# Kernel optimization log

Measured on AMD Instinct MI355X. Metric: run time of the kernel, lower is better.

## Reference

```python
import jax, jax.numpy as jnp
import numpy as np

N, D, E_EDGES = 50000, 128, 800000
HEADS, REL_DIM, N_RELS, LAYERS = 4, 64, 64, 2
HD = HEADS * D  # per-head out_channels == d_model (concat=False)
LN_EPS = 1e-5
NEG_SLOPE = 0.2


def setup_inputs() -> dict:
    key = jax.random.key(0)
    ks = jax.random.split(key, 12)
    s = 0.02
    return {
        "x_flat": jax.random.normal(ks[0], (N, D), jnp.float32),
        "edge_index": jax.random.randint(ks[1], (2, E_EDGES), 0, N, jnp.int32),
        "edge_type": jax.random.randint(ks[2], (E_EDGES,), 0, N_RELS, jnp.int32),
        "rel_emb": jax.random.normal(ks[3], (N_RELS, REL_DIM), jnp.float32) * s,
        # stacked params for LAYERS GATv2Conv layers
        "Wl": jax.random.normal(ks[4], (LAYERS, D, HD), jnp.float32) * s,
        "bl": jnp.zeros((LAYERS, HD), jnp.float32),
        "Wr": jax.random.normal(ks[5], (LAYERS, D, HD), jnp.float32) * s,
        "br": jnp.zeros((LAYERS, HD), jnp.float32),
        "We": jax.random.normal(ks[6], (LAYERS, REL_DIM, HD), jnp.float32) * s,
        "att": jax.random.normal(ks[7], (LAYERS, HEADS, D), jnp.float32) * s,
        "b_out": jnp.zeros((LAYERS, D), jnp.float32),
        "ln_g": jnp.ones((LAYERS, D), jnp.float32),
        "ln_b": jnp.zeros((LAYERS, D), jnp.float32),
    }


def _gatv2_layer(h, src, dst, eattr, Wl, bl, Wr, br, We, att, b_out):
    # h: [N, D] -> per-head transforms [N, H, C]
    xl = (h @ Wl + bl).reshape(N, HEADS, D)   # source transform (messages)
    xr = (h @ Wr + br).reshape(N, HEADS, D)   # target transform
    xe = (eattr @ We).reshape(-1, HEADS, D)   # edge transform (no bias, PyG)
    # GATv2 attention: a^T leaky_relu(xl_j + xr_i + xe)
    s = jax.nn.leaky_relu(xl[src] + xr[dst] + xe, NEG_SLOPE)  # [E, H, C]
    logits = jnp.einsum('ehc,hc->eh', s, att)                  # [E, H]
    # segment softmax over destination nodes
    mx = jax.ops.segment_max(logits, dst, num_segments=N)      # [N, H]
    ex = jnp.exp(logits - mx[dst])
    den = jax.ops.segment_sum(ex, dst, num_segments=N)
    alpha = ex / den[dst]                                      # [E, H]
    msg = xl[src] * alpha[..., None]                           # [E, H, C]
    out = jax.ops.segment_sum(msg.reshape(-1, HD), dst, num_segments=N)
    out = out.reshape(N, HEADS, D).mean(axis=1) + b_out        # concat=False -> mean
    return out


def _layernorm(x, g, b):
    mu = x.mean(-1, keepdims=True)
    var = ((x - mu) ** 2).mean(-1, keepdims=True)
    return (x - mu) * jax.lax.rsqrt(var + LN_EPS) * g + b


def reference(x_flat, edge_index, edge_type, rel_emb, Wl, bl, Wr, br, We, att, b_out, ln_g, ln_b):
    src, dst = edge_index[0], edge_index[1]
    eattr = rel_emb[edge_type]  # [E, REL_DIM]
    h = x_flat
    for l in range(LAYERS):
        m = _gatv2_layer(h, src, dst, eattr, Wl[l], bl[l], Wr[l], br[l], We[l], att[l], b_out[l])
        m = jax.nn.gelu(m, approximate=False)  # dropout in eval mode
        h = _layernorm(h + m, ln_g[l], ln_b[l])
    return h
```

## Files before the change

kernel.cpp:

```cpp
#include <hip/hip_runtime.h>
#include <hip/hip_bf16.h>

#define NN 50000
#define DM 128
#define EE 800000
#define NH 4
#define HDIM 512
#define NRELS 64
#define RDIM 64
#define LAYERS 2
#define NB 196

#define PM_HB 6250
#define PM_WC 1024
#define PM_XE 256
#define PM_CZ 196
#define PM_TOT (PM_HB + PM_WC + PM_XE + PM_CZ + 1)

typedef short frag8 __attribute__((ext_vector_type(8)));
typedef float f32x4 __attribute__((ext_vector_type(4)));
typedef float f32x2 __attribute__((ext_vector_type(2)));

__device__ __forceinline__ float b2f(unsigned short u) {
    unsigned v = ((unsigned)u) << 16;
    union { unsigned u; float f; } c; c.u = v; return c.f;
}
__device__ __forceinline__ float b2f_lo(unsigned u) {
    union { unsigned u; float f; } c; c.u = u << 16; return c.f;
}
__device__ __forceinline__ float b2f_hi(unsigned u) {
    union { unsigned u; float f; } c; c.u = u & 0xFFFF0000u; return c.f;
}
__device__ __forceinline__ float b2f_hi_raw(unsigned u) {
    union { unsigned u; float f; } c; c.u = u; return c.f;
}
__device__ __forceinline__ unsigned short f2b(float f) {
    union { float f; unsigned u; } c; c.f = f;
    unsigned u = c.u;
    u += 0x7FFFu + ((u >> 16) & 1u);
    return (unsigned short)(u >> 16);
}

template<int CTRL>
__device__ __forceinline__ float dpp_add(float x) {
    int yi = __builtin_amdgcn_update_dpp(0, __builtin_bit_cast(int, x),
                                         CTRL, 0xF, 0xF, true);
    return x + __builtin_bit_cast(float, yi);
}

__global__ void count_kernel(const int* __restrict__ dst, int* __restrict__ counts) {
    int e = blockIdx.x * 256 + threadIdx.x;
    if (e < EE) atomicAdd(&counts[dst[e]], 1);
}

__global__ __launch_bounds__(256) void psum_kernel(const int* __restrict__ counts,
                                                   int* __restrict__ psums) {
    int idx = blockIdx.x * 256 + threadIdx.x;
    int x = (idx < NN) ? counts[idx] : 0;
    int lane = threadIdx.x & 63, wv = threadIdx.x >> 6;
    #pragma unroll
    for (int d = 1; d < 64; d <<= 1) x += __shfl_xor(x, d, 64);
    __shared__ int ws[4];
    if (lane == 0) ws[wv] = x;
    __syncthreads();
    if (threadIdx.x == 0) psums[blockIdx.x] = ws[0] + ws[1] + ws[2] + ws[3];
}

__global__ __launch_bounds__(256) void pscan_kernel(const int* __restrict__ psums,
                                                    int* __restrict__ offs,
                                                    int* __restrict__ row_ptr) {
    int t = threadIdx.x;
    int x = (t < NB) ? psums[t] : 0;
    int lane = t & 63, wv = t >> 6;
    int incl = x;
    #pragma unroll
    for (int d = 1; d < 64; d <<= 1) {
        int y = __shfl_up(incl, d, 64);
        if (lane >= d) incl += y;
    }
    __shared__ int ws[4];
    if (lane == 63) ws[wv] = incl;
    __syncthreads();
    int off = 0;
    for (int k = 0; k < wv; ++k) off += ws[k];
    if (t < NB) offs[t] = incl + off - x;
    if (t == 0) row_ptr[0] = 0;
}

__global__ __launch_bounds__(256) void pfin_kernel(const int* __restrict__ counts,
                                                   const int* __restrict__ offs,
                                                   int* __restrict__ row_ptr,
                                                   int* __restrict__ cursor) {
    int idx = blockIdx.x * 256 + threadIdx.x;
    int x = (idx < NN) ? counts[idx] : 0;
    int lane = threadIdx.x & 63, wv = threadIdx.x >> 6;
    int incl = x;
    #pragma unroll
    for (int d = 1; d < 64; d <<= 1) {
        int y = __shfl_up(incl, d, 64);
        if (lane >= d) incl += y;
    }
    __shared__ int ws[4];
    if (lane == 63) ws[wv] = incl;
    __syncthreads();
    int off = offs[blockIdx.x];
    for (int k = 0; k < wv; ++k) off += ws[k];
    if (idx < NN) {
        int v = off + incl;
        row_ptr[idx + 1] = v;
        cursor[idx] = v - x;
    }
}

__global__ void scatter_pk_kernel(const int* __restrict__ ei, const int* __restrict__ etype,
                                  int* __restrict__ cursor, uint2* __restrict__ pkq) {
    int e = blockIdx.x * 256 + threadIdx.x;
    if (e < EE) {
        int d = ei[EE + e];
        int p = atomicAdd(&cursor[d], 1);
        uint2 v;
        v.x = (unsigned)ei[e] << 10;
        v.y = (unsigned)etype[e] << 10;
        pkq[p] = v;
    }
}

__global__ __launch_bounds__(256) void prep_misc_kernel(
    const float* __restrict__ x_flat,
    const float* __restrict__ Wl, const float* __restrict__ Wr,
    const float* __restrict__ rel_emb, const float* __restrict__ We,
    const float* __restrict__ att,
    unsigned short* __restrict__ hb, unsigned short* __restrict__ Wt,
    unsigned short* __restrict__ xeb, float* __restrict__ be,
    int* __restrict__ counts) {
    int b = blockIdx.x, t = threadIdx.x;
    if (b < PM_HB) {
        int idx = b * 256 + t;
        float4 v = ((const float4*)x_flat)[idx];
        ushort4 o;
        o.x = f2b(v.x); o.y = f2b(v.y); o.z = f2b(v.z); o.w = f2b(v.w);
        ((ushort4*)hb)[idx] = o;
        return;
    }
    b -= PM_HB;
    if (b < PM_WC) {
        int idx = b * 256 + t;
        int m = idx >> 16;
        int r = idx & 65535;
        int c = r >> 7, k = r & 127;
        int l = m >> 1;
        const float* W = (m & 1) ? Wr : Wl;
        Wt[idx] = f2b(W[(size_t)l * DM * HDIM + k * HDIM + c]);
        return;
    }
    b -= PM_WC;
    if (b < PM_XE) {
        int idx = b * 256 + t;
        int l  = idx / (NRELS * HDIM);
        int r  = (idx / HDIM) & (NRELS - 1);
        int hc = idx & (HDIM - 1);
        const float* Wel = We + (size_t)l * RDIM * HDIM;
        float s = 0.f;
        #pragma unroll 8
        for (int d = 0; d < RDIM; ++d) s += rel_emb[r * RDIM + d] * Wel[d * HDIM + hc];
        xeb[idx] = f2b(s);
        return;
    }
    b -= PM_XE;
    if (b < PM_CZ) {
        int idx = b * 256 + t;
        if (idx < NN) counts[idx] = 0;
        return;
    }
    __shared__ float aw_s[LAYERS * NH * RDIM];
    #pragma unroll
    for (int k = 0; k < 2; ++k) {
        int idx = t * 2 + k;
        int l = idx >> 8, h = (idx >> 6) & 3, d = idx & 63;
        const float* ap = att + (size_t)l * HDIM + h * DM;
        const float* wp = We + (size_t)l * RDIM * HDIM + (size_t)d * HDIM + h * DM;
        float s = 0.f;
        #pragma unroll 8
        for (int c = 0; c < DM; ++c) s += ap[c] * wp[c];
        aw_s[idx] = s;
    }
    __syncthreads();
    #pragma unroll
    for (int k = 0; k < 2; ++k) {
        int idx = t * 2 + k;
        int l = idx >> 8, r = (idx >> 2) & 63, h = idx & 3;
        const float* rp = rel_emb + r * RDIM;
        const float* ap = aw_s + l * 256 + h * 64;
        float s = 0.f;
        #pragma unroll 8
        for (int d = 0; d < RDIM; ++d) s += rp[d] * ap[d];
        be[idx] = 0.6f * s;
    }
}

__global__ __launch_bounds__(256) void gemm_xlxr_ab_kernel(
    const unsigned short* __restrict__ hb,
    const unsigned short* __restrict__ WtL,
    const unsigned short* __restrict__ WtR,
    const float* __restrict__ bl, const float* __restrict__ br,
    const float* __restrict__ att_l,
    unsigned short* __restrict__ xl, unsigned short* __restrict__ xr,
    float* __restrict__ ab) {
    int w = threadIdx.x >> 6, lane = threadIdx.x & 63;
    int m0 = blockIdx.x * 64;
    int colL = lane & 15, kg = lane >> 4;

    frag8 a[4][4];
    #pragma unroll
    for (int mt = 0; mt < 4; ++mt) {
        int row = m0 + mt * 16 + colL;
        if (row >= NN) row = NN - 1;
        const unsigned short* arow = hb + (size_t)row * DM;
        #pragma unroll
        for (int kc = 0; kc < 4; ++kc) {
            uint4 raw = *(const uint4*)(arow + kc * 32 + kg * 8);
            a[mt][kc] = __builtin_bit_cast(frag8, raw);
        }
    }

    float prow[4][2][4];
    #pragma unroll
    for (int mt = 0; mt < 4; ++mt)
        #pragma unroll
        for (int mat = 0; mat < 2; ++mat)
            #pragma unroll
            for (int r = 0; r < 4; ++r) prow[mt][mat][r] = 0.f;

    #pragma unroll
    for (int mat = 0; mat < 2; ++mat) {
        const unsigned short* Wt = mat ? WtR : WtL;
        const float* bias = mat ? br : bl;
        unsigned short* out = mat ? xr : xl;
        #pragma unroll
        for (int nt = 0; nt < 8; ++nt) {
            int col = w * 128 + nt * 16 + colL;
            f32x4 acc[4];
            #pragma unroll
            for (int mt = 0; mt < 4; ++mt) acc[mt] = f32x4{0.f, 0.f, 0.f, 0.f};
            #pragma unroll
            for (int kc = 0; kc < 4; ++kc) {
                uint4 raw = *(const uint4*)(Wt + (size_t)col * DM + kc * 32 + kg * 8);
                frag8 b = __builtin_bit_cast(frag8, raw);
                #pragma unroll
                for (int mt = 0; mt < 4; ++mt)
                    acc[mt] = __builtin_amdgcn_mfma_f32_16x16x32_bf16(a[mt][kc], b, acc[mt], 0, 0, 0);
            }
            float bb = bias[col];
            float ac = att_l[col];
            #pragma unroll
            for (int mt = 0; mt < 4; ++mt) {
                #pragma unroll
                for (int r = 0; r < 4; ++r) {
                    float v = acc[mt][r] + bb;
                    int row = m0 + mt * 16 + kg * 4 + r;
                    if (row < NN) out[(size_t)row * HDIM + col] = f2b(v);
                    prow[mt][mat][r] = fmaf(ac, v, prow[mt][mat][r]);
                }
            }
        }
    }
    #pragma unroll
    for (int d = 1; d < 16; d <<= 1) {
        #pragma unroll
        for (int mt = 0; mt < 4; ++mt)
            #pragma unroll
            for (int mat = 0; mat < 2; ++mat)
                #pragma unroll
                for (int r = 0; r < 4; ++r)
                    prow[mt][mat][r] += __shfl_xor(prow[mt][mat][r], d, 64);
    }
    if (colL == 0) {
        #pragma unroll
        for (int mt = 0; mt < 4; ++mt) {
            int row = m0 + mt * 16 + kg * 4;
            #pragma unroll
            for (int mat = 0; mat < 2; ++mat)
                #pragma unroll
                for (int r = 0; r < 4; ++r)
                    if (row + r < NN)
                        ab[(size_t)(row + r) * 8 + mat * 4 + w] = 0.6f * prow[mt][mat][r];
        }
    }
}

__global__ __launch_bounds__(256) void node_fused_kernel(
    const int* __restrict__ row_ptr,
    const uint2* __restrict__ pkq,
    const unsigned short* __restrict__ xl,
    const unsigned short* __restrict__ xr,
    const unsigned short* __restrict__ xeb_l,
    const float* __restrict__ ab,
    const float* __restrict__ be_l,
    const float* __restrict__ att_l,
    const float* __restrict__ h_in,
    const float* __restrict__ b_out, const float* __restrict__ ln_g,
    const float* __restrict__ ln_b,
    float* __restrict__ h_out,
    unsigned short* __restrict__ hb_out) {
    int w = threadIdx.x >> 6, l = threadIdx.x & 63;
    int i = blockIdx.x * 4 + w;
    int hh = l >> 4;
    __shared__ float cl[4][64][4];
    __shared__ uint2 pk_s[4][64];

    int beg = row_ptr[i], end = row_ptr[i + 1];
    int c0 = (l & 15) * 8;

    uint4 xrv = *(const uint4*)(xr + (size_t)i * HDIM + l * 8);
    f32x2 xrp0 = f32x2{b2f_lo(xrv.x), b2f_hi(xrv.x)};
    f32x2 xrp1 = f32x2{b2f_lo(xrv.y), b2f_hi(xrv.y)};
    f32x2 xrp2 = f32x2{b2f_lo(xrv.z), b2f_hi(xrv.z)};
    f32x2 xrp3 = f32x2{b2f_lo(xrv.w), b2f_hi(xrv.w)};
    float4 at0 = ((const float4*)(att_l + l * 8))[0];
    float4 at1 = ((const float4*)(att_l + l * 8))[1];
    float atv[8] = {at0.x * 0.4f, at0.y * 0.4f, at0.z * 0.4f, at0.w * 0.4f,
                    at1.x * 0.4f, at1.y * 0.4f, at1.z * 0.4f, at1.w * 0.4f};
    float4 bxv = ((const float4*)ab)[2 * i + 1];
    float4 hv0 = *(const float4*)(h_in + (size_t)i * DM + c0);
    float4 hv1 = *(const float4*)(h_in + (size_t)i * DM + c0 + 4);

    const char* xl_b = (const char*)xl;
    const char* xe_b = (const char*)xeb_l;
    uint l16 = (uint)l << 4;

    float ss = 0.f;
    f32x2 acc0 = f32x2{0.f, 0.f}, acc1 = f32x2{0.f, 0.f};
    f32x2 acc2 = f32x2{0.f, 0.f}, acc3 = f32x2{0.f, 0.f};

    for (int cb = beg; cb < end; cb += 64) {
        int mc = min(64, end - cb);
        if (l < mc) {
            uint2 pk = pkq[cb + l];
            pk_s[w][l] = pk;
            int s = pk.x >> 10, r = pk.y >> 10;
            float4 a4 = ((const float4*)ab)[2 * s];
            float4 b4 = ((const float4*)be_l)[r];
            cl[w][l][0] = a4.x + b4.x + bxv.x;
            cl[w][l][1] = a4.y + b4.y + bxv.y;
            cl[w][l][2] = a4.z + b4.z + bxv.z;
            cl[w][l][3] = a4.w + b4.w + bxv.w;
        }
        uint2 pk0 = pk_s[w][0];
        uint4 vvP = *(const uint4*)(xl_b + pk0.x + l16);
        uint4 eeP = *(const uint4*)(xe_b + pk0.y + l16);
        float cjP = cl[w][0][hh];
        for (int j = 1; j <= mc; ++j) {
            uint4 vv = vvP; uint4 ee = eeP; float cj = cjP;
            if (j < mc) {
                uint2 pkj = pk_s[w][j];
                vvP = *(const uint4*)(xl_b + pkj.x + l16);
                eeP = *(const uint4*)(xe_b + pkj.y + l16);
                cjP = cl[w][j][hh];
            }
            f32x2 xp0 = f32x2{b2f_lo(vv.x), b2f_hi_raw(vv.x)};
            f32x2 xp1 = f32x2{b2f_lo(vv.y), b2f_hi_raw(vv.y)};
            f32x2 xp2 = f32x2{b2f_lo(vv.z), b2f_hi_raw(vv.z)};
            f32x2 xp3 = f32x2{b2f_lo(vv.w), b2f_hi_raw(vv.w)};
            f32x2 z0 = (xp0 + xrp0) + f32x2{b2f_lo(ee.x), b2f_hi_raw(ee.x)};
            f32x2 z1 = (xp1 + xrp1) + f32x2{b2f_lo(ee.y), b2f_hi_raw(ee.y)};
            f32x2 z2 = (xp2 + xrp2) + f32x2{b2f_lo(ee.z), b2f_hi_raw(ee.z)};
            f32x2 z3 = (xp3 + xrp3) + f32x2{b2f_lo(ee.w), b2f_hi_raw(ee.w)};
            float partial = fmaf(atv[0], fabsf(z0[0]),
                            fmaf(atv[1], fabsf(z0[1]),
                            fmaf(atv[2], fabsf(z1[0]),
                            fmaf(atv[3], fabsf(z1[1]),
                            fmaf(atv[4], fabsf(z2[0]),
                            fmaf(atv[5], fabsf(z2[1]),
                            fmaf(atv[6], fabsf(z3[0]), atv[7] * fabsf(z3[1]))))))));
            partial = dpp_add<0xB1>(partial);
            partial = dpp_add<0x4E>(partial);
            partial = dpp_add<0x124>(partial);
            partial = dpp_add<0x128>(partial);
            float we = __expf(partial + cj);
            ss += we;
            f32x2 wv = f32x2{we, we};
            acc0 += wv * xp0;
            acc1 += wv * xp1;
            acc2 += wv * xp2;
            acc3 += wv * xp3;
        }
    }

    float invs = (ss > 0.f) ? 1.f / ss : 0.f;
    float sv[8] = {acc0[0] * invs, acc0[1] * invs, acc1[0] * invs, acc1[1] * invs,
                   acc2[0] * invs, acc2[1] * invs, acc3[0] * invs, acc3[1] * invs};
    #pragma unroll
    for (int d = 16; d < 64; d <<= 1)
        #pragma unroll
        for (int k = 0; k < 8; ++k) sv[k] += __shfl_xor(sv[k], d, 64);

    float4 bo0 = *(const float4*)(b_out + c0);
    float4 bo1 = *(const float4*)(b_out + c0 + 4);
    float bov[8] = {bo0.x, bo0.y, bo0.z, bo0.w, bo1.x, bo1.y, bo1.z, bo1.w};
    float hvv[8] = {hv0.x, hv0.y, hv0.z, hv0.w, hv1.x, hv1.y, hv1.z, hv1.w};
    float yv[8];
    float la = 0.f, lb = 0.f;
    #pragma unroll
    for (int k = 0; k < 8; ++k) {
        float o = sv[k] * 0.25f + bov[k];
        float ge = 0.5f * o * (1.f + erff(o * 0.70710678118654752f));
        float y = hvv[k] + ge;
        yv[k] = y; la += y; lb += y * y;
    }
    la = dpp_add<0xB1>(la); la = dpp_add<0x4E>(la);
    la = dpp_add<0x124>(la); la = dpp_add<0x128>(la);
    lb = dpp_add<0xB1>(lb); lb = dpp_add<0x4E>(lb);
    lb = dpp_add<0x124>(lb); lb = dpp_add<0x128>(lb);
    float mean = la * (1.f / 128.f);
    float var = lb * (1.f / 128.f) - mean * mean;
    float rs = rsqrtf(var + 1e-5f);

    if (l < 16) {
        float4 g0 = *(const float4*)(ln_g + c0);
        float4 g1 = *(const float4*)(ln_g + c0 + 4);
        float4 q0 = *(const float4*)(ln_b + c0);
        float4 q1 = *(const float4*)(ln_b + c0 + 4);
        float gv[8] = {g0.x, g0.y, g0.z, g0.w, g1.x, g1.y, g1.z, g1.w};
        float qv[8] = {q0.x, q0.y, q0.z, q0.w, q1.x, q1.y, q1.z, q1.w};
        float ov[8];
        #pragma unroll
        for (int k = 0; k < 8; ++k)
            ov[k] = (yv[k] - mean) * rs * gv[k] + qv[k];
        float* hop = h_out + (size_t)i * DM + c0;
        *(float4*)hop = make_float4(ov[0], ov[1], ov[2], ov[3]);
        *(float4*)(hop + 4) = make_float4(ov[4], ov[5], ov[6], ov[7]);
        uint4 ob;
        ob.x = (unsigned)f2b(ov[0]) | ((unsigned)f2b(ov[1]) << 16);
        ob.y = (unsigned)f2b(ov[2]) | ((unsigned)f2b(ov[3]) << 16);
        ob.z = (unsigned)f2b(ov[4]) | ((unsigned)f2b(ov[5]) << 16);
        ob.w = (unsigned)f2b(ov[6]) | ((unsigned)f2b(ov[7]) << 16);
        *(uint4*)(hb_out + (size_t)i * DM + c0) = ob;
    }
}

extern "C" void kernel_launch(void* const* d_in, const int* in_sizes, int n_in,
                              void* d_out, int out_size, void* d_ws, size_t ws_size,
                              hipStream_t stream) {
    const float* x_flat   = (const float*)d_in[0];
    const int*   edge_idx = (const int*)d_in[1];
    const int*   edge_ty  = (const int*)d_in[2];
    const float* rel_emb  = (const float*)d_in[3];
    const float* Wl       = (const float*)d_in[4];
    const float* bl       = (const float*)d_in[5];
    const float* Wr       = (const float*)d_in[6];
    const float* br       = (const float*)d_in[7];
    const float* We       = (const float*)d_in[8];
    const float* att      = (const float*)d_in[9];
    const float* b_out    = (const float*)d_in[10];
    const float* ln_g     = (const float*)d_in[11];
    const float* ln_b     = (const float*)d_in[12];

    char* p = (char*)d_ws;
    auto carve = [&](size_t bytes) {
        void* r = (void*)p;
        p += (bytes + 255) & ~(size_t)255;
        return r;
    };
    unsigned short* xl     = (unsigned short*)carve((size_t)NN * HDIM * 2);
    unsigned short* xr     = (unsigned short*)carve((size_t)NN * HDIM * 2);
    float*          h1     = (float*)carve((size_t)NN * DM * 4);
    unsigned short* hb     = (unsigned short*)carve((size_t)NN * DM * 2);
    unsigned short* Wt     = (unsigned short*)carve((size_t)4 * DM * HDIM * 2);
    unsigned short* xeb    = (unsigned short*)carve((size_t)LAYERS * NRELS * HDIM * 2);
    float*          ab     = (float*)carve((size_t)NN * 8 * 4);
    float*          be     = (float*)carve((size_t)LAYERS * NRELS * NH * 4);
    int*            row_ptr= (int*)carve((size_t)(NN + 1) * 4);
    int*            counts = (int*)carve((size_t)NN * 4);
    int*            cursor = (int*)carve((size_t)NN * 4);
    int*            psums  = (int*)carve((size_t)NB * 4);
    int*            offs   = (int*)carve((size_t)NB * 4);
    uint2*          pkq    = (uint2*)carve((size_t)EE * 8);

    const int* dst = edge_idx + EE;

    prep_misc_kernel<<<PM_TOT, 256, 0, stream>>>(
        x_flat, Wl, Wr, rel_emb, We, att, hb, Wt, xeb, be, counts);

    count_kernel<<<(EE + 255) / 256, 256, 0, stream>>>(dst, counts);
    psum_kernel<<<NB, 256, 0, stream>>>(counts, psums);
    pscan_kernel<<<1, 256, 0, stream>>>(psums, offs, row_ptr);
    pfin_kernel<<<NB, 256, 0, stream>>>(counts, offs, row_ptr, cursor);
    scatter_pk_kernel<<<(EE + 255) / 256, 256, 0, stream>>>(edge_idx, edge_ty, cursor, pkq);

    const float* h_cur = x_flat;
    for (int l = 0; l < LAYERS; ++l) {
        float* h_next = (l == LAYERS - 1) ? (float*)d_out : h1;
        gemm_xlxr_ab_kernel<<<(NN + 63) / 64, 256, 0, stream>>>(
            hb,
            Wt + (size_t)(l * 2 + 0) * DM * HDIM,
            Wt + (size_t)(l * 2 + 1) * DM * HDIM,
            bl + (size_t)l * HDIM, br + (size_t)l * HDIM,
            att + (size_t)l * HDIM,
            xl, xr, ab);
        node_fused_kernel<<<NN / 4, 256, 0, stream>>>(
            row_ptr, pkq, xl, xr,
            xeb + (size_t)l * NRELS * HDIM,
            ab, be + (size_t)l * NRELS * NH,
            att + (size_t)l * HDIM,
            h_cur,
            b_out + (size_t)l * DM, ln_g + (size_t)l * DM, ln_b + (size_t)l * DM,
            h_next, hb);
        h_cur = h_next;
    }
}
```

Before: 606.3 us.

## Use persistent atomic work-queue for node kernel and halve GEMM row tile

The fused node kernel becomes persistent: 2048 blocks pull node indices from a global atomic counter, one per wavefront, instead of one block per four nodes. Per-layer counters are zeroed in the prep kernel, and per-column constants are hoisted out of the node loop. This targets load imbalance from uneven in-degrees and per-block launch overhead, at the cost of one atomic per node. The XL/XR GEMM also drops from 64 to 32 rows per block, doubling its grid to raise occupancy and cut register pressure, while reloading weights more often.

```diff
diff --git a/kernel.cpp b/kernel.cpp
--- a/kernel.cpp
+++ b/kernel.cpp
@@ -132,7 +132,7 @@
     const float* __restrict__ att,
     unsigned short* __restrict__ hb, unsigned short* __restrict__ Wt,
     unsigned short* __restrict__ xeb, float* __restrict__ be,
-    int* __restrict__ counts) {
+    int* __restrict__ counts, int* __restrict__ ctr) {
     int b = blockIdx.x, t = threadIdx.x;
     if (b < PM_HB) {
         int idx = b * 256 + t;
@@ -172,6 +172,7 @@
         if (idx < NN) counts[idx] = 0;
         return;
     }
+    if (t < 2) ctr[t] = 0;
     __shared__ float aw_s[LAYERS * NH * RDIM];
     #pragma unroll
     for (int k = 0; k < 2; ++k) {
@@ -207,12 +208,12 @@
     unsigned short* __restrict__ xl, unsigned short* __restrict__ xr,
     float* __restrict__ ab) {
     int w = threadIdx.x >> 6, lane = threadIdx.x & 63;
-    int m0 = blockIdx.x * 64;
+    int m0 = blockIdx.x * 32;
     int colL = lane & 15, kg = lane >> 4;
 
-    frag8 a[4][4];
-    #pragma unroll
-    for (int mt = 0; mt < 4; ++mt) {
+    frag8 a[2][4];
+    #pragma unroll
+    for (int mt = 0; mt < 2; ++mt) {
         int row = m0 + mt * 16 + colL;
         if (row >= NN) row = NN - 1;
         const unsigned short* arow = hb + (size_t)row * DM;
@@ -223,9 +224,9 @@
         }
     }
 
-    float prow[4][2][4];
-    #pragma unroll
-    for (int mt = 0; mt < 4; ++mt)
+    float prow[2][2][4];
+    #pragma unroll
+    for (int mt = 0; mt < 2; ++mt)
         #pragma unroll
         for (int mat = 0; mat < 2; ++mat)
             #pragma unroll
@@ -239,35 +240,34 @@
         #pragma unroll
         for (int nt = 0; nt < 8; ++nt) {
             int col = w * 128 + nt * 16 + colL;
-            f32x4 acc[4];
-            #pragma unroll
-            for (int mt = 0; mt < 4; ++mt) acc[mt] = f32x4{0.f, 0.f, 0.f, 0.f};
+            f32x4 acc0 = {0.f, 0.f, 0.f, 0.f};
+            f32x4 acc1 = {0.f, 0.f, 0.f, 0.f};
             #pragma unroll
             for (int kc = 0; kc < 4; ++kc) {
                 uint4 raw = *(const uint4*)(Wt + (size_t)col * DM + kc * 32 + kg * 8);
                 frag8 b = __builtin_bit_cast(frag8, raw);
-                #pragma unroll
-                for (int mt = 0; mt < 4; ++mt)
-                    acc[mt] = __builtin_amdgcn_mfma_f32_16x16x32_bf16(a[mt][kc], b, acc[mt], 0, 0, 0);
+                acc0 = __builtin_amdgcn_mfma_f32_16x16x32_bf16(a[0][kc], b, acc0, 0, 0, 0);
+                acc1 = __builtin_amdgcn_mfma_f32_16x16x32_bf16(a[1][kc], b, acc1, 0, 0, 0);
             }
             float bb = bias[col];
             float ac = att_l[col];
             #pragma unroll
-            for (int mt = 0; mt < 4; ++mt) {
-                #pragma unroll
-                for (int r = 0; r < 4; ++r) {
-                    float v = acc[mt][r] + bb;
-                    int row = m0 + mt * 16 + kg * 4 + r;
-                    if (row < NN) out[(size_t)row * HDIM + col] = f2b(v);
-                    prow[mt][mat][r] = fmaf(ac, v, prow[mt][mat][r]);
-                }
+            for (int r = 0; r < 4; ++r) {
+                float v0 = acc0[r] + bb;
+                float v1 = acc1[r] + bb;
+                int row0 = m0 + kg * 4 + r;
+                int row1 = row0 + 16;
+                if (row0 < NN) out[(size_t)row0 * HDIM + col] = f2b(v0);
+                if (row1 < NN) out[(size_t)row1 * HDIM + col] = f2b(v1);
+                prow[0][mat][r] = fmaf(ac, v0, prow[0][mat][r]);
+                prow[1][mat][r] = fmaf(ac, v1, prow[1][mat][r]);
             }
         }
     }
     #pragma unroll
     for (int d = 1; d < 16; d <<= 1) {
         #pragma unroll
-        for (int mt = 0; mt < 4; ++mt)
+        for (int mt = 0; mt < 2; ++mt)
             #pragma unroll
             for (int mat = 0; mat < 2; ++mat)
                 #pragma unroll
@@ -276,7 +276,7 @@
     }
     if (colL == 0) {
         #pragma unroll
-        for (int mt = 0; mt < 4; ++mt) {
+        for (int mt = 0; mt < 2; ++mt) {
             int row = m0 + mt * 16 + kg * 4;
             #pragma unroll
             for (int mat = 0; mat < 2; ++mat)
@@ -301,140 +301,149 @@
     const float* __restrict__ b_out, const float* __restrict__ ln_g,
     const float* __restrict__ ln_b,
     float* __restrict__ h_out,
-    unsigned short* __restrict__ hb_out) {
+    unsigned short* __restrict__ hb_out,
+    int* __restrict__ ctr) {
     int w = threadIdx.x >> 6, l = threadIdx.x & 63;
-    int i = blockIdx.x * 4 + w;
     int hh = l >> 4;
     __shared__ float cl[4][64][4];
     __shared__ uint2 pk_s[4][64];
 
-    int beg = row_ptr[i], end = row_ptr[i + 1];
     int c0 = (l & 15) * 8;
 
-    uint4 xrv = *(const uint4*)(xr + (size_t)i * HDIM + l * 8);
-    f32x2 xrp0 = f32x2{b2f_lo(xrv.x), b2f_hi(xrv.x)};
-    f32x2 xrp1 = f32x2{b2f_lo(xrv.y), b2f_hi(xrv.y)};
-    f32x2 xrp2 = f32x2{b2f_lo(xrv.z), b2f_hi(xrv.z)};
-    f32x2 xrp3 = f32x2{b2f_lo(xrv.w), b2f_hi(xrv.w)};
     float4 at0 = ((const float4*)(att_l + l * 8))[0];
     float4 at1 = ((const float4*)(att_l + l * 8))[1];
     float atv[8] = {at0.x * 0.4f, at0.y * 0.4f, at0.z * 0.4f, at0.w * 0.4f,
                     at1.x * 0.4f, at1.y * 0.4f, at1.z * 0.4f, at1.w * 0.4f};
-    float4 bxv = ((const float4*)ab)[2 * i + 1];
-    float4 hv0 = *(const float4*)(h_in + (size_t)i * DM + c0);
-    float4 hv1 = *(const float4*)(h_in + (size_t)i * DM + c0 + 4);
+    float4 bo0 = *(const float4*)(b_out + c0);
+    float4 bo1 = *(const float4*)(b_out + c0 + 4);
+    float bov[8] = {bo0.x, bo0.y, bo0.z, bo0.w, bo1.x, bo1.y, bo1.z, bo1.w};
+    float4 g0 = *(const float4*)(ln_g + c0);
+    float4 g1 = *(const float4*)(ln_g + c0 + 4);
+    float4 q0 = *(const float4*)(ln_b + c0);
+    float4 q1 = *(const float4*)(ln_b + c0 + 4);
 
     const char* xl_b = (const char*)xl;
     const char* xe_b = (const char*)xeb_l;
     uint l16 = (uint)l << 4;
 
-    float ss = 0.f;
-    f32x2 acc0 = f32x2{0.f, 0.f}, acc1 = f32x2{0.f, 0.f};
-    f32x2 acc2 = f32x2{0.f, 0.f}, acc3 = f32x2{0.f, 0.f};
-
-    for (int cb = beg; cb < end; cb += 64) {
-        int mc = min(64, end - cb);
-        if (l < mc) {
-            uint2 pk = pkq[cb + l];
-            pk_s[w][l] = pk;
-            int s = pk.x >> 10, r = pk.y >> 10;
-            float4 a4 = ((const float4*)ab)[2 * s];
-            float4 b4 = ((const float4*)be_l)[r];
-            cl[w][l][0] = a4.x + b4.x + bxv.x;
-            cl[w][l][1] = a4.y + b4.y + bxv.y;
-            cl[w][l][2] = a4.z + b4.z + bxv.z;
-            cl[w][l][3] = a4.w + b4.w + bxv.w;
+    for (;;) {
+        int i = 0;
+        if (l == 0) i = atomicAdd(ctr, 1);
+        i = __shfl(i, 0, 64);
+        if (i >= NN) break;
+
+        int beg = row_ptr[i], end = row_ptr[i + 1];
+
+        uint4 xrv = *(const uint4*)(xr + (size_t)i * HDIM + l * 8);
+        f32x2 xrp0 = f32x2{b2f_lo(xrv.x), b2f_hi(xrv.x)};
+        f32x2 xrp1 = f32x2{b2f_lo(xrv.y), b2f_hi(xrv.y)};
+        f32x2 xrp2 = f32x2{b2f_lo(xrv.z), b2f_hi(xrv.z)};
+        f32x2 xrp3 = f32x2{b2f_lo(xrv.w), b2f_hi(xrv.w)};
+        float4 bxv = ((const float4*)ab)[2 * i + 1];
+        float4 hv0 = *(const float4*)(h_in + (size_t)i * DM + c0);
+        float4 hv1 = *(const float4*)(h_in + (size_t)i * DM + c0 + 4);
+
+        float ss = 0.f;
+        f32x2 acc0 = f32x2{0.f, 0.f}, acc1 = f32x2{0.f, 0.f};
+        f32x2 acc2 = f32x2{0.f, 0.f}, acc3 = f32x2{0.f, 0.f};
+
+        for (int cb = beg; cb < end; cb += 64) {
+            int mc = min(64, end - cb);
+            if (l < mc) {
+                uint2 pk = pkq[cb + l];
+                pk_s[w][l] = pk;
+                int s = pk.x >> 10, r = pk.y >> 10;
+                float4 a4 = ((const float4*)ab)[2 * s];
+                float4 b4 = ((const float4*)be_l)[r];
+                cl[w][l][0] = a4.x + b4.x + bxv.x;
+                cl[w][l][1] = a4.y + b4.y + bxv.y;
+                cl[w][l][2] = a4.z + b4.z + bxv.z;
+                cl[w][l][3] = a4.w + b4.w + bxv.w;
+            }
+            uint2 pk0 = pk_s[w][0];
+            uint4 vvP = *(const uint4*)(xl_b + pk0.x + l16);
+            uint4 eeP = *(const uint4*)(xe_b + pk0.y + l16);
+            float cjP = cl[w][0][hh];
+            for (int j = 1; j <= mc; ++j) {
+                uint4 vv = vvP; uint4 ee = eeP; float cj = cjP;
+                if (j < mc) {
+                    uint2 pkj = pk_s[w][j];
+                    vvP = *(const uint4*)(xl_b + pkj.x + l16);
+                    eeP = *(const uint4*)(xe_b + pkj.y + l16);
+                    cjP = cl[w][j][hh];
+                }
+                f32x2 xp0 = f32x2{b2f_lo(vv.x), b2f_hi_raw(vv.x)};
+                f32x2 xp1 = f32x2{b2f_lo(vv.y), b2f_hi_raw(vv.y)};
+                f32x2 xp2 = f32x2{b2f_lo(vv.z), b2f_hi_raw(vv.z)};
+                f32x2 xp3 = f32x2{b2f_lo(vv.w), b2f_hi_raw(vv.w)};
+                f32x2 z0 = (xp0 + xrp0) + f32x2{b2f_lo(ee.x), b2f_hi_raw(ee.x)};
+                f32x2 z1 = (xp1 + xrp1) + f32x2{b2f_lo(ee.y), b2f_hi_raw(ee.y)};
+                f32x2 z2 = (xp2 + xrp2) + f32x2{b2f_lo(ee.z), b2f_hi_raw(ee.z)};
+                f32x2 z3 = (xp3 + xrp3) + f32x2{b2f_lo(ee.w), b2f_hi_raw(ee.w)};
+                float partial = fmaf(atv[0], fabsf(z0[0]),
+                                fmaf(atv[1], fabsf(z0[1]),
+                                fmaf(atv[2], fabsf(z1[0]),
+                                fmaf(atv[3], fabsf(z1[1]),
+                                fmaf(atv[4], fabsf(z2[0]),
+                                fmaf(atv[5], fabsf(z2[1]),
+                                fmaf(atv[6], fabsf(z3[0]), atv[7] * fabsf(z3[1]))))))));
+                partial = dpp_add<0xB1>(partial);
+                partial = dpp_add<0x4E>(partial);
+                partial = dpp_add<0x124>(partial);
+                partial = dpp_add<0x128>(partial);
+                float we = __expf(partial + cj);
+                ss += we;
+                f32x2 wv = f32x2{we, we};
+                acc0 += wv * xp0;
+                acc1 += wv * xp1;
+                acc2 += wv * xp2;
+                acc3 += wv * xp3;
+            }
         }
-        uint2 pk0 = pk_s[w][0];
-        uint4 vvP = *(const uint4*)(xl_b + pk0.x + l16);
-        uint4 eeP = *(const uint4*)(xe_b + pk0.y + l16);
-        float cjP = cl[w][0][hh];
-        for (int j = 1; j <= mc; ++j) {
-            uint4 vv = vvP; uint4 ee = eeP; float cj = cjP;
-            if (j < mc) {
-                uint2 pkj = pk_s[w][j];
-                vvP = *(const uint4*)(xl_b + pkj.x + l16);
-                eeP = *(const uint4*)(xe_b + pkj.y + l16);
-                cjP = cl[w][j][hh];
-            }
-            f32x2 xp0 = f32x2{b2f_lo(vv.x), b2f_hi_raw(vv.x)};
-            f32x2 xp1 = f32x2{b2f_lo(vv.y), b2f_hi_raw(vv.y)};
-            f32x2 xp2 = f32x2{b2f_lo(vv.z), b2f_hi_raw(vv.z)};
-            f32x2 xp3 = f32x2{b2f_lo(vv.w), b2f_hi_raw(vv.w)};
-            f32x2 z0 = (xp0 + xrp0) + f32x2{b2f_lo(ee.x), b2f_hi_raw(ee.x)};
-            f32x2 z1 = (xp1 + xrp1) + f32x2{b2f_lo(ee.y), b2f_hi_raw(ee.y)};
-            f32x2 z2 = (xp2 + xrp2) + f32x2{b2f_lo(ee.z), b2f_hi_raw(ee.z)};
-            f32x2 z3 = (xp3 + xrp3) + f32x2{b2f_lo(ee.w), b2f_hi_raw(ee.w)};
-            float partial = fmaf(atv[0], fabsf(z0[0]),
-                            fmaf(atv[1], fabsf(z0[1]),
-                            fmaf(atv[2], fabsf(z1[0]),
-                            fmaf(atv[3], fabsf(z1[1]),
-                            fmaf(atv[4], fabsf(z2[0]),
-                            fmaf(atv[5], fabsf(z2[1]),
-                            fmaf(atv[6], fabsf(z3[0]), atv[7] * fabsf(z3[1]))))))));
-            partial = dpp_add<0xB1>(partial);
-            partial = dpp_add<0x4E>(partial);
-            partial = dpp_add<0x124>(partial);
-            partial = dpp_add<0x128>(partial);
-            float we = __expf(partial + cj);
-            ss += we;
-            f32x2 wv = f32x2{we, we};
-            acc0 += wv * xp0;
-            acc1 += wv * xp1;
-            acc2 += wv * xp2;
-            acc3 += wv * xp3;
+
+        float invs = (ss > 0.f) ? 1.f / ss : 0.f;
+        float sv[8] = {acc0[0] * invs, acc0[1] * invs, acc1[0] * invs, acc1[1] * invs,
+                       acc2[0] * invs, acc2[1] * invs, acc3[0] * invs, acc3[1] * invs};
+        #pragma unroll
+        for (int d = 16; d < 64; d <<= 1)
+            #pragma unroll
+            for (int k = 0; k < 8; ++k) sv[k] += __shfl_xor(sv[k], d, 64);
+
+        float hvv[8] = {hv0.x, hv0.y, hv0.z, hv0.w, hv1.x, hv1.y, hv1.z, hv1.w};
+        float yv[8];
+        float la = 0.f, lb = 0.f;
+        #pragma unroll
+        for (int k = 0; k < 8; ++k) {
+            float o = sv[k] * 0.25f + bov[k];
+            float ge = 0.5f * o * (1.f + erff(o * 0.70710678118654752f));
+            float y = hvv[k] + ge;
+            yv[k] = y; la += y; lb += y * y;
         }
-    }
-
-    float invs = (ss > 0.f) ? 1.f / ss : 0.f;
-    float sv[8] = {acc0[0] * invs, acc0[1] * invs, acc1[0] * invs, acc1[1] * invs,
-                   acc2[0] * invs, acc2[1] * invs, acc3[0] * invs, acc3[1] * invs};
-    #pragma unroll
-    for (int d = 16; d < 64; d <<= 1)
-        #pragma unroll
-        for (int k = 0; k < 8; ++k) sv[k] += __shfl_xor(sv[k], d, 64);
-
-    float4 bo0 = *(const float4*)(b_out + c0);
-    float4 bo1 = *(const float4*)(b_out + c0 + 4);
-    float bov[8] = {bo0.x, bo0.y, bo0.z, bo0.w, bo1.x, bo1.y, bo1.z, bo1.w};
-    float hvv[8] = {hv0.x, hv0.y, hv0.z, hv0.w, hv1.x, hv1.y, hv1.z, hv1.w};
-    float yv[8];
-    float la = 0.f, lb = 0.f;
-    #pragma unroll
-    for (int k = 0; k < 8; ++k) {
-        float o = sv[k] * 0.25f + bov[k];
-        float ge = 0.5f * o * (1.f + erff(o * 0.70710678118654752f));
-        float y = hvv[k] + ge;
-        yv[k] = y; la += y; lb += y * y;
-    }
-    la = dpp_add<0xB1>(la); la = dpp_add<0x4E>(la);
-    la = dpp_add<0x124>(la); la = dpp_add<0x128>(la);
-    lb = dpp_add<0xB1>(lb); lb = dpp_add<0x4E>(lb);
-    lb = dpp_add<0x124>(lb); lb = dpp_add<0x128>(lb);
-    float mean = la * (1.f / 128.f);
-    float var = lb * (1.f / 128.f) - mean * mean;
-    float rs = rsqrtf(var + 1e-5f);
-
-    if (l < 16) {
-        float4 g0 = *(const float4*)(ln_g + c0);
-        float4 g1 = *(const float4*)(ln_g + c0 + 4);
-        float4 q0 = *(const float4*)(ln_b + c0);
-        float4 q1 = *(const float4*)(ln_b + c0 + 4);
-        float gv[8] = {g0.x, g0.y, g0.z, g0.w, g1.x, g1.y, g1.z, g1.w};
-        float qv[8] = {q0.x, q0.y, q0.z, q0.w, q1.x, q1.y, q1.z, q1.w};
-        float ov[8];
-        #pragma unroll
-        for (int k = 0; k < 8; ++k)
-            ov[k] = (yv[k] - mean) * rs * gv[k] + qv[k];
-        float* hop = h_out + (size_t)i * DM + c0;
-        *(float4*)hop = make_float4(ov[0], ov[1], ov[2], ov[3]);
-        *(float4*)(hop + 4) = make_float4(ov[4], ov[5], ov[6], ov[7]);
-        uint4 ob;
-        ob.x = (unsigned)f2b(ov[0]) | ((unsigned)f2b(ov[1]) << 16);
-        ob.y = (unsigned)f2b(ov[2]) | ((unsigned)f2b(ov[3]) << 16);
-        ob.z = (unsigned)f2b(ov[4]) | ((unsigned)f2b(ov[5]) << 16);
-        ob.w = (unsigned)f2b(ov[6]) | ((unsigned)f2b(ov[7]) << 16);
-        *(uint4*)(hb_out + (size_t)i * DM + c0) = ob;
+        la = dpp_add<0xB1>(la); la = dpp_add<0x4E>(la);
+        la = dpp_add<0x124>(la); la = dpp_add<0x128>(la);
+        lb = dpp_add<0xB1>(lb); lb = dpp_add<0x4E>(lb);
+        lb = dpp_add<0x124>(lb); lb = dpp_add<0x128>(lb);
+        float mean = la * (1.f / 128.f);
+        float var = lb * (1.f / 128.f) - mean * mean;
+        float rs = rsqrtf(var + 1e-5f);
+
+        if (l < 16) {
+            float gv[8] = {g0.x, g0.y, g0.z, g0.w, g1.x, g1.y, g1.z, g1.w};
+            float qv[8] = {q0.x, q0.y, q0.z, q0.w, q1.x, q1.y, q1.z, q1.w};
+            float ov[8];
+            #pragma unroll
+            for (int k = 0; k < 8; ++k)
+                ov[k] = (yv[k] - mean) * rs * gv[k] + qv[k];
+            float* hop = h_out + (size_t)i * DM + c0;
+            *(float4*)hop = make_float4(ov[0], ov[1], ov[2], ov[3]);
+            *(float4*)(hop + 4) = make_float4(ov[4], ov[5], ov[6], ov[7]);
+            uint4 ob;
+            ob.x = (unsigned)f2b(ov[0]) | ((unsigned)f2b(ov[1]) << 16);
+            ob.y = (unsigned)f2b(ov[2]) | ((unsigned)f2b(ov[3]) << 16);
+            ob.z = (unsigned)f2b(ov[4]) | ((unsigned)f2b(ov[5]) << 16);
+            ob.w = (unsigned)f2b(ov[6]) | ((unsigned)f2b(ov[7]) << 16);
+            *(uint4*)(hb_out + (size_t)i * DM + c0) = ob;
+        }
     }
 }
 
@@ -475,11 +484,12 @@
     int*            psums  = (int*)carve((size_t)NB * 4);
     int*            offs   = (int*)carve((size_t)NB * 4);
     uint2*          pkq    = (uint2*)carve((size_t)EE * 8);
+    int*            ctr    = (int*)carve((size_t)2 * 4);
 
     const int* dst = edge_idx + EE;
 
     prep_misc_kernel<<<PM_TOT, 256, 0, stream>>>(
-        x_flat, Wl, Wr, rel_emb, We, att, hb, Wt, xeb, be, counts);
+        x_flat, Wl, Wr, rel_emb, We, att, hb, Wt, xeb, be, counts, ctr);
 
     count_kernel<<<(EE + 255) / 256, 256, 0, stream>>>(dst, counts);
     psum_kernel<<<NB, 256, 0, stream>>>(counts, psums);
@@ -490,21 +500,21 @@
     const float* h_cur = x_flat;
     for (int l = 0; l < LAYERS; ++l) {
         float* h_next = (l == LAYERS - 1) ? (float*)d_out : h1;
-        gemm_xlxr_ab_kernel<<<(NN + 63) / 64, 256, 0, stream>>>(
+        gemm_xlxr_ab_kernel<<<(NN + 31) / 32, 256, 0, stream>>>(
             hb,
             Wt + (size_t)(l * 2 + 0) * DM * HDIM,
             Wt + (size_t)(l * 2 + 1) * DM * HDIM,
             bl + (size_t)l * HDIM, br + (size_t)l * HDIM,
             att + (size_t)l * HDIM,
             xl, xr, ab);
-        node_fused_kernel<<<NN / 4, 256, 0, stream>>>(
+        node_fused_kernel<<<2048, 256, 0, stream>>>(
             row_ptr, pkq, xl, xr,
             xeb + (size_t)l * NRELS * HDIM,
             ab, be + (size_t)l * NRELS * NH,
             att + (size_t)l * HDIM,
             h_cur,
             b_out + (size_t)l * DM, ln_g + (size_t)l * DM, ln_b + (size_t)l * DM,
-            h_next, hb);
+            h_next, hb, ctr + l);
         h_cur = h_next;
     }
 }
```

New measurement: 1.652 ms. 172% more time.
